# Kernel optimization log

Hardware: AMD Instinct MI355X
Metric: run time of the kernel (lower is better)

Reference implementation:

```python
import jax, jax.numpy as jnp
import numpy as np

B, S, D = 8, 1024, 1024
H, DH = 16, 64  # num_attention_heads, attention_head_size; H*DH == D


def setup_inputs() -> dict:
    key = jax.random.key(0)
    ks = jax.random.split(key, 6)
    scale = 0.02
    return {
        "hidden_states": jax.random.normal(ks[0], (B, S, D), jnp.float32),
        "right_hidden_states": jax.random.normal(ks[1], (B, S, D), jnp.float32),
        "attention_mask": jnp.ones((B, S, S), jnp.float32),
        "Wq": jax.random.normal(ks[2], (D, H * DH), jnp.float32) * scale,
        "bq": jnp.zeros((H * DH,), jnp.float32),
        "Wk": jax.random.normal(ks[3], (D, H * DH), jnp.float32) * scale,
        "bk": jnp.zeros((H * DH,), jnp.float32),
        "Wv": jax.random.normal(ks[4], (D, H * DH), jnp.float32) * scale,
        "bv": jnp.zeros((H * DH,), jnp.float32),
    }


def _split_heads(x, b):
    # (B, S, H*DH) -> (B, H, S, DH)
    return x.reshape(b, -1, H, DH).transpose(0, 2, 1, 3)


def reference(hidden_states, right_hidden_states, attention_mask, Wq, bq, Wk, bk, Wv, bv):
    b = hidden_states.shape[0]
    q = _split_heads(hidden_states @ Wq + bq, b)          # (B,H,Sq,DH)
    k = _split_heads(right_hidden_states @ Wk + bk, b)    # (B,H,Sk,DH)
    v = _split_heads(right_hidden_states @ Wv + bv, b)    # (B,H,Sk,DH)

    scores = jnp.einsum("bhqd,bhkd->bhqk", q, k) / jnp.sqrt(jnp.asarray(DH, q.dtype))
    scores = jnp.sum(scores, axis=1, keepdims=True)       # (B,1,Sq,Sk) head-summed

    ext = (1.0 - attention_mask[:, None, :, :].astype(scores.dtype)) * -1e9
    probs = jax.nn.softmax(scores + ext, axis=-1)         # (B,1,Sq,Sk)

    ctx = jnp.matmul(probs, v)                            # broadcast -> (B,H,Sq,DH)
    # Faithful to original: reshape WITHOUT transposing heads back.
    return ctx.reshape(b, -1, H * DH)                     # (B,Sq,H*DH)
```

## Files before the change

kernel.cpp:

```cpp
#include <hip/hip_runtime.h>
#include <stdint.h>

constexpr int S = 1024;
constexpr int D = 1024;
constexpr int NB = 8;

typedef __bf16 bf16x8 __attribute__((ext_vector_type(8)));
typedef float floatx4 __attribute__((ext_vector_type(4)));

#define AS1 __attribute__((address_space(1)))
#define AS3 __attribute__((address_space(3)))

__device__ __forceinline__ unsigned short f2bf(float f) {
  unsigned u = __builtin_bit_cast(unsigned, f);
  u += 0x7fffu + ((u >> 16) & 1u);
  return (unsigned short)(u >> 16);
}

__device__ __forceinline__ void gload16(const void* g, void* l) {
  __builtin_amdgcn_global_load_lds((const AS1 unsigned int*)g, (AS3 unsigned int*)l, 16, 0, 0);
}

__global__ __launch_bounds__(256) void prep_kernel(const float4* __restrict__ hs4,
                                                   const float4* __restrict__ rhs4,
                                                   ushort4* __restrict__ hsb4,
                                                   ushort4* __restrict__ rhsb4, int n4,
                                                   const float* __restrict__ Wq,
                                                   const float* __restrict__ Wk,
                                                   const float* __restrict__ Wv,
                                                   unsigned short* __restrict__ Wcat) {
  __shared__ float tile[32][33];
  const int bid = blockIdx.x;
  if (bid < 16384) {
    int i = bid * 256 + threadIdx.x;
    const float4* src;
    ushort4* dst;
    int j;
    if (i < n4) {
      src = hs4; dst = hsb4; j = i;
    } else {
      src = rhs4; dst = rhsb4; j = i - n4;
    }
    float4 v = src[j];
    ushort4 o;
    o.x = f2bf(v.x); o.y = f2bf(v.y); o.z = f2bf(v.z); o.w = f2bf(v.w);
    dst[j] = o;
  } else {
    const int t = bid - 16384;
    const int z = t >> 10;
    const int r = t & 1023;
    const float* W = (z == 0) ? Wq : (z == 1) ? Wk : Wv;
    unsigned short* Wt = Wcat + (long long)z * D * D;
    const int bx = (r & 31) * 32;
    const int by = (r >> 5) * 32;
    const int x = threadIdx.x & 31;
    const int y0 = threadIdx.x >> 5;
    for (int i = 0; i < 4; ++i) {
      int y = y0 + i * 8;
      tile[y][x] = W[(by + y) * D + bx + x];
    }
    __syncthreads();
    for (int i = 0; i < 4; ++i) {
      int y = y0 + i * 8;
      Wt[(long long)(bx + y) * D + by + x] = f2bf(tile[x][y]);
    }
  }
}


__global__ __launch_bounds__(256) void gemm_qkv_kernel(
    const unsigned short* __restrict__ hsb, const unsigned short* __restrict__ rhsb,
    const unsigned short* __restrict__ Wcat, unsigned short* __restrict__ Qm,
    unsigned short* __restrict__ Km, unsigned short* __restrict__ Vmt,
    const float* __restrict__ bq, const float* __restrict__ bk, const float* __restrict__ bv) {
  __shared__ __align__(16) unsigned short As[128 * 64];
  __shared__ __align__(16) unsigned short Bs[128 * 64];
  const int tid = threadIdx.x;
  const int lane = tid & 63;
  const int w = tid >> 6;
  const int bid = blockIdx.x;
  const int local = bid >> 3;
  const int n_tile = (bid & 7) * 3 + (local % 3);
  const long long m0 = (long long)(local / 3) * 128;
  const long long n0g = (long long)n_tile * 128;
  const int seg = n_tile >> 3;
  const unsigned short* A = (seg == 0) ? hsb : rhsb;
  const unsigned short* Bt = Wcat + n0g * D;
  const float* bias = (seg == 0) ? bq : (seg == 1) ? bk : bv;

  const unsigned short* aG[4];
  const unsigned short* bG[4];
  for (int j = 0; j < 4; ++j) {
    int idx = tid + j * 256;
    int row = idx >> 3;
    int cg = (idx & 7) ^ (row & 7);
    aG[j] = A + (m0 + row) * D + cg * 8;
    bG[j] = Bt + (long long)row * D + cg * 8;
  }

  floatx4 zero4 = {0.f, 0.f, 0.f, 0.f};
  floatx4 acc[4][4];
  for (int i = 0; i < 4; ++i)
    for (int j = 0; j < 4; ++j) acc[i][j] = zero4;

  const int r15 = lane & 15;
  const int quad = lane >> 4;
  const int wm = (w >> 1) * 64;
  const int wn = (w & 1) * 64;

  for (int k0 = 0; k0 < D; k0 += 64) {
    for (int j = 0; j < 4; ++j) gload16(aG[j] + k0, As + j * 2048 + w * 512);
    for (int j = 0; j < 4; ++j) gload16(bG[j] + k0, Bs + j * 2048 + w * 512);
    __syncthreads();
    for (int kk = 0; kk < 2; ++kk) {
      const int ca = ((kk << 2) | quad) ^ (r15 & 7);
      bf16x8 af[4], bfr[4];
      for (int t = 0; t < 4; ++t) {
        af[t] = *reinterpret_cast<const bf16x8*>(As + (wm + t * 16 + r15) * 64 + ca * 8);
        bfr[t] = *reinterpret_cast<const bf16x8*>(Bs + (wn + t * 16 + r15) * 64 + ca * 8);
      }
      for (int mt = 0; mt < 4; ++mt)
        for (int nt = 0; nt < 4; ++nt)
          acc[mt][nt] =
              __builtin_amdgcn_mfma_f32_16x16x32_bf16(af[mt], bfr[nt], acc[mt][nt], 0, 0, 0);
    }
    __syncthreads();
  }

  const long long nloc0 = n0g & 1023;
  for (int mt = 0; mt < 4; ++mt) {
    for (int nt = 0; nt < 4; ++nt) {
      const long long mrow = m0 + wm + mt * 16 + quad * 4;
      const long long nc = nloc0 + wn + nt * 16 + r15;
      const float bval = bias[nc];
      floatx4 v = acc[mt][nt];
      for (int e = 0; e < 4; ++e) {
        float val = v[e] + bval;
        long long m = mrow + e;
        if (seg == 0) {
          Qm[m * D + nc] = f2bf(val);
        } else if (seg == 1) {
          Km[m * D + nc] = f2bf(val);
        } else {
          Vmt[(m >> 10) * (long long)(S * D) + nc * S + (m & 1023)] = f2bf(val);
        }
      }
    }
  }
}

template <int MODE>
__global__ __launch_bounds__(256) void gemm_nt_kernel(
    const unsigned short* __restrict__ A, int lda, long long strideA,
    const unsigned short* __restrict__ Bt, int ldb, long long strideB, float* __restrict__ C,
    long long strideC, float alpha, int K) {
  __shared__ __align__(16) unsigned short As[128 * 64];
  __shared__ __align__(16) unsigned short Bs[128 * 64];
  const int tid = threadIdx.x;
  const int lane = tid & 63;
  const int w = tid >> 6;
  const int bid = blockIdx.x;
  const int z = bid & 7;
  const int local = bid >> 3;
  const long long m0 = (long long)(local & 7) * 128;
  const long long n0 = (long long)(local >> 3) * 128;
  A += (long long)z * strideA;
  Bt += (long long)z * strideB;

  const unsigned short* aG[4];
  const unsigned short* bG[4];
  for (int j = 0; j < 4; ++j) {
    int idx = tid + j * 256;
    int row = idx >> 3;
    int cg = (idx & 7) ^ (row & 7);
    aG[j] = A + (m0 + row) * lda + cg * 8;
    bG[j] = Bt + (n0 + row) * ldb + cg * 8;
  }

  floatx4 zero4 = {0.f, 0.f, 0.f, 0.f};
  floatx4 acc[4][4];
  for (int i = 0; i < 4; ++i)
    for (int j = 0; j < 4; ++j) acc[i][j] = zero4;

  const int r15 = lane & 15;
  const int quad = lane >> 4;
  const int wm = (w >> 1) * 64;
  const int wn = (w & 1) * 64;

  for (int k0 = 0; k0 < K; k0 += 64) {
    for (int j = 0; j < 4; ++j) gload16(aG[j] + k0, As + j * 2048 + w * 512);
    for (int j = 0; j < 4; ++j) gload16(bG[j] + k0, Bs + j * 2048 + w * 512);
    __syncthreads();
    for (int kk = 0; kk < 2; ++kk) {
      const int ca = ((kk << 2) | quad) ^ (r15 & 7);
      bf16x8 af[4], bfr[4];
      for (int t = 0; t < 4; ++t) {
        af[t] = *reinterpret_cast<const bf16x8*>(As + (wm + t * 16 + r15) * 64 + ca * 8);
        bfr[t] = *reinterpret_cast<const bf16x8*>(Bs + (wn + t * 16 + r15) * 64 + ca * 8);
      }
      for (int mt = 0; mt < 4; ++mt)
        for (int nt = 0; nt < 4; ++nt)
          acc[mt][nt] =
              __builtin_amdgcn_mfma_f32_16x16x32_bf16(af[mt], bfr[nt], acc[mt][nt], 0, 0, 0);
    }
    __syncthreads();
  }

  for (int mt = 0; mt < 4; ++mt) {
    for (int nt = 0; nt < 4; ++nt) {
      const long long mrow = m0 + wm + mt * 16 + quad * 4;
      const long long ncol = n0 + wn + nt * 16 + r15;
      floatx4 v = acc[mt][nt];
      for (int e = 0; e < 4; ++e) {
        float val = v[e] * alpha;
        long long m = mrow + e;
        if constexpr (MODE == 2) {
          C[(long long)z * strideC + m * S + ncol] = val;
        } else {
          C[(long long)z * strideC + (ncol >> 6) * (long long)(S * 64) + m * 64 + (ncol & 63)] =
              val;
        }
      }
    }
  }
}

__global__ __launch_bounds__(256) void softmax_kernel(const float* scores,
                                                      const float* __restrict__ mask,
                                                      unsigned short* probs) {
  const int bid = blockIdx.x;
  const long long row = (long long)(bid & 7) * 1024 + (bid >> 3);
  const float4* s4 = (const float4*)(scores + row * S);
  const float4* m4 = (const float4*)(mask + row * S);
  ushort4* p4 = (ushort4*)(probs + row * 2048);
  const int tid = threadIdx.x;
  const int lane = tid & 63, w = tid >> 6;
  float4 sv = s4[tid];
  float4 mv = m4[tid];
  float v[4] = {sv.x + (1.0f - mv.x) * -1e9f, sv.y + (1.0f - mv.y) * -1e9f,
                sv.z + (1.0f - mv.z) * -1e9f, sv.w + (1.0f - mv.w) * -1e9f};
  float mx = fmaxf(fmaxf(v[0], v[1]), fmaxf(v[2], v[3]));
  for (int off = 32; off; off >>= 1) mx = fmaxf(mx, __shfl_xor(mx, off, 64));
  __shared__ float redm[4], reds[4];
  if (lane == 0) redm[w] = mx;
  __syncthreads();
  mx = fmaxf(fmaxf(redm[0], redm[1]), fmaxf(redm[2], redm[3]));
  float sum = 0.f;
  for (int i = 0; i < 4; ++i) {
    v[i] = __expf(v[i] - mx);
    sum += v[i];
  }
  for (int off = 32; off; off >>= 1) sum += __shfl_xor(sum, off, 64);
  if (lane == 0) reds[w] = sum;
  __syncthreads();
  sum = reds[0] + reds[1] + reds[2] + reds[3];
  float inv = 1.0f / sum;
  ushort4 o;
  o.x = f2bf(v[0] * inv);
  o.y = f2bf(v[1] * inv);
  o.z = f2bf(v[2] * inv);
  o.w = f2bf(v[3] * inv);
  p4[tid] = o;
}

extern "C" void kernel_launch(void* const* d_in, const int* in_sizes, int n_in, void* d_out,
                              int out_size, void* d_ws, size_t ws_size, hipStream_t stream) {
  const float* hs = (const float*)d_in[0];
  const float* rhs = (const float*)d_in[1];
  const float* mask = (const float*)d_in[2];
  const float* Wq = (const float*)d_in[3];
  const float* bq = (const float*)d_in[4];
  const float* Wk = (const float*)d_in[5];
  const float* bk = (const float*)d_in[6];
  const float* Wv = (const float*)d_in[7];
  const float* bv = (const float*)d_in[8];
  float* out = (float*)d_out;
  char* ws = (char*)d_ws;
  const size_t MB = 1ull << 20;
  unsigned short* Wcat = (unsigned short*)(ws + 0 * MB);
  unsigned short* hsb = (unsigned short*)(ws + 6 * MB);
  unsigned short* rhsb = (unsigned short*)(ws + 22 * MB);
  unsigned short* Qm = (unsigned short*)(ws + 38 * MB);
  unsigned short* Km = (unsigned short*)(ws + 54 * MB);
  unsigned short* Vmt = (unsigned short*)(ws + 70 * MB);
  float* scores = (float*)(ws + 6 * MB);
  unsigned short* probs = (unsigned short*)scores;

  const int n4 = NB * S * D / 4;
  prep_kernel<<<16384 + 3072, 256, 0, stream>>>((const float4*)hs, (const float4*)rhs,
                                                (ushort4*)hsb, (ushort4*)rhsb, n4, Wq, Wk, Wv,
                                                Wcat);

  gemm_qkv_kernel<<<1536, 256, 0, stream>>>(hsb, rhsb, Wcat, Qm, Km, Vmt, bq, bk, bv);

  gemm_nt_kernel<2><<<512, 256, 0, stream>>>(Qm, D, (long long)S * D, Km, D, (long long)S * D,
                                             scores, (long long)S * S, 0.125f, D);
  softmax_kernel<<<NB * S, 256, 0, stream>>>(scores, mask, probs);
  gemm_nt_kernel<3><<<512, 256, 0, stream>>>(probs, 2048, (long long)S * 2048, Vmt, D,
                                             (long long)S * D, out, (long long)S * D, 1.f, D);
}
```

Baseline: 304.2 us.

## Register-prefetch GEMM tiles with K=32 stages instead of direct global-to-LDS loads

Both GEMM kernels drop the global_load_lds direct copies and instead load the next K=32 slice into registers while the current slice is computed, then store it into a smaller swizzled LDS buffer. The goal is to overlap global latency with MFMA work and halve LDS footprint, which can raise occupancy. In exchange there are twice as many barriers per K, extra VGPR use and a register round trip through LDS stores. The swizzle layout also changes, packing two rows per 64-element LDS line.

```diff
diff --git a/kernel.cpp b/kernel.cpp
--- a/kernel.cpp
+++ b/kernel.cpp
@@ -7,18 +7,12 @@
 
 typedef __bf16 bf16x8 __attribute__((ext_vector_type(8)));
 typedef float floatx4 __attribute__((ext_vector_type(4)));
-
-#define AS1 __attribute__((address_space(1)))
-#define AS3 __attribute__((address_space(3)))
+typedef unsigned short ushort8v __attribute__((ext_vector_type(8)));
 
 __device__ __forceinline__ unsigned short f2bf(float f) {
   unsigned u = __builtin_bit_cast(unsigned, f);
   u += 0x7fffu + ((u >> 16) & 1u);
   return (unsigned short)(u >> 16);
-}
-
-__device__ __forceinline__ void gload16(const void* g, void* l) {
-  __builtin_amdgcn_global_load_lds((const AS1 unsigned int*)g, (AS3 unsigned int*)l, 16, 0, 0);
 }
 
 __global__ __launch_bounds__(256) void prep_kernel(const float4* __restrict__ hs4,
@@ -68,13 +62,32 @@
 }
 
 
+#define GEMM_STAGE_ADDRS(Abase, lda_, Bbase, ldb_)                           \
+  const int srow0 = (tid >> 3) * 2 + ((tid >> 2) & 1);                       \
+  const int scol0 = (tid & 3) * 8;                                           \
+  const unsigned short* aG0 = (Abase) + (long long)(srow0) * (lda_) + scol0; \
+  const unsigned short* aG1 = aG0 + (long long)64 * (lda_);                  \
+  const unsigned short* bG0 = (Bbase) + (long long)(srow0) * (ldb_) + scol0; \
+  const unsigned short* bG1 = bG0 + (long long)64 * (ldb_);                  \
+  const int sr0 = tid >> 3;                                                  \
+  const int w0 = sr0 * 64 + (((tid & 7) ^ (sr0 & 7)) * 8);                   \
+  const int sr1 = sr0 + 32;                                                  \
+  const int w1 = sr1 * 64 + (((tid & 7) ^ (sr1 & 7)) * 8);
+
+#define GEMM_FRAG_READ(dst, Buf, wbase)                                      \
+  for (int t = 0; t < 4; ++t) {                                              \
+    int sr = ((wbase) + t * 16) / 2 + (r15 >> 1);                            \
+    int ch = p4q ^ (sr & 7);                                                 \
+    dst[t] = *reinterpret_cast<const bf16x8*>(Buf + sr * 64 + ch * 8);       \
+  }
+
 __global__ __launch_bounds__(256) void gemm_qkv_kernel(
     const unsigned short* __restrict__ hsb, const unsigned short* __restrict__ rhsb,
     const unsigned short* __restrict__ Wcat, unsigned short* __restrict__ Qm,
     unsigned short* __restrict__ Km, unsigned short* __restrict__ Vmt,
     const float* __restrict__ bq, const float* __restrict__ bk, const float* __restrict__ bv) {
-  __shared__ __align__(16) unsigned short As[128 * 64];
-  __shared__ __align__(16) unsigned short Bs[128 * 64];
+  __shared__ __align__(16) unsigned short As[128 * 32];
+  __shared__ __align__(16) unsigned short Bs[128 * 32];
   const int tid = threadIdx.x;
   const int lane = tid & 63;
   const int w = tid >> 6;
@@ -84,19 +97,11 @@
   const long long m0 = (long long)(local / 3) * 128;
   const long long n0g = (long long)n_tile * 128;
   const int seg = n_tile >> 3;
-  const unsigned short* A = (seg == 0) ? hsb : rhsb;
+  const unsigned short* A = ((seg == 0) ? hsb : rhsb) + m0 * D;
   const unsigned short* Bt = Wcat + n0g * D;
   const float* bias = (seg == 0) ? bq : (seg == 1) ? bk : bv;
 
-  const unsigned short* aG[4];
-  const unsigned short* bG[4];
-  for (int j = 0; j < 4; ++j) {
-    int idx = tid + j * 256;
-    int row = idx >> 3;
-    int cg = (idx & 7) ^ (row & 7);
-    aG[j] = A + (m0 + row) * D + cg * 8;
-    bG[j] = Bt + (long long)row * D + cg * 8;
-  }
+  GEMM_STAGE_ADDRS(A, D, Bt, D)
 
   floatx4 zero4 = {0.f, 0.f, 0.f, 0.f};
   floatx4 acc[4][4];
@@ -105,26 +110,32 @@
 
   const int r15 = lane & 15;
   const int quad = lane >> 4;
+  const int p4q = (r15 & 1) * 4 + quad;
   const int wm = (w >> 1) * 64;
   const int wn = (w & 1) * 64;
 
-  for (int k0 = 0; k0 < D; k0 += 64) {
-    for (int j = 0; j < 4; ++j) gload16(aG[j] + k0, As + j * 2048 + w * 512);
-    for (int j = 0; j < 4; ++j) gload16(bG[j] + k0, Bs + j * 2048 + w * 512);
-    __syncthreads();
-    for (int kk = 0; kk < 2; ++kk) {
-      const int ca = ((kk << 2) | quad) ^ (r15 & 7);
-      bf16x8 af[4], bfr[4];
-      for (int t = 0; t < 4; ++t) {
-        af[t] = *reinterpret_cast<const bf16x8*>(As + (wm + t * 16 + r15) * 64 + ca * 8);
-        bfr[t] = *reinterpret_cast<const bf16x8*>(Bs + (wn + t * 16 + r15) * 64 + ca * 8);
-      }
-      for (int mt = 0; mt < 4; ++mt)
-        for (int nt = 0; nt < 4; ++nt)
-          acc[mt][nt] =
-              __builtin_amdgcn_mfma_f32_16x16x32_bf16(af[mt], bfr[nt], acc[mt][nt], 0, 0, 0);
-    }
-    __syncthreads();
+  ushort8v sA0 = *(const ushort8v*)aG0, sA1 = *(const ushort8v*)aG1;
+  ushort8v sB0 = *(const ushort8v*)bG0, sB1 = *(const ushort8v*)bG1;
+  for (int k0 = 0; k0 < D; k0 += 32) {
+    __syncthreads();
+    *(ushort8v*)(As + w0) = sA0;
+    *(ushort8v*)(As + w1) = sA1;
+    *(ushort8v*)(Bs + w0) = sB0;
+    *(ushort8v*)(Bs + w1) = sB1;
+    __syncthreads();
+    if (k0 + 32 < D) {
+      sA0 = *(const ushort8v*)(aG0 + k0 + 32);
+      sA1 = *(const ushort8v*)(aG1 + k0 + 32);
+      sB0 = *(const ushort8v*)(bG0 + k0 + 32);
+      sB1 = *(const ushort8v*)(bG1 + k0 + 32);
+    }
+    bf16x8 af[4], bfr[4];
+    GEMM_FRAG_READ(af, As, wm)
+    GEMM_FRAG_READ(bfr, Bs, wn)
+    for (int mt = 0; mt < 4; ++mt)
+      for (int nt = 0; nt < 4; ++nt)
+        acc[mt][nt] =
+            __builtin_amdgcn_mfma_f32_16x16x32_bf16(af[mt], bfr[nt], acc[mt][nt], 0, 0, 0);
   }
 
   const long long nloc0 = n0g & 1023;
@@ -154,8 +165,8 @@
     const unsigned short* __restrict__ A, int lda, long long strideA,
     const unsigned short* __restrict__ Bt, int ldb, long long strideB, float* __restrict__ C,
     long long strideC, float alpha, int K) {
-  __shared__ __align__(16) unsigned short As[128 * 64];
-  __shared__ __align__(16) unsigned short Bs[128 * 64];
+  __shared__ __align__(16) unsigned short As[128 * 32];
+  __shared__ __align__(16) unsigned short Bs[128 * 32];
   const int tid = threadIdx.x;
   const int lane = tid & 63;
   const int w = tid >> 6;
@@ -164,18 +175,10 @@
   const int local = bid >> 3;
   const long long m0 = (long long)(local & 7) * 128;
   const long long n0 = (long long)(local >> 3) * 128;
-  A += (long long)z * strideA;
-  Bt += (long long)z * strideB;
-
-  const unsigned short* aG[4];
-  const unsigned short* bG[4];
-  for (int j = 0; j < 4; ++j) {
-    int idx = tid + j * 256;
-    int row = idx >> 3;
-    int cg = (idx & 7) ^ (row & 7);
-    aG[j] = A + (m0 + row) * lda + cg * 8;
-    bG[j] = Bt + (n0 + row) * ldb + cg * 8;
-  }
+  const unsigned short* Ab = A + (long long)z * strideA + m0 * lda;
+  const unsigned short* Bb = Bt + (long long)z * strideB + n0 * ldb;
+
+  GEMM_STAGE_ADDRS(Ab, lda, Bb, ldb)
 
   floatx4 zero4 = {0.f, 0.f, 0.f, 0.f};
   floatx4 acc[4][4];
@@ -184,26 +187,32 @@
 
   const int r15 = lane & 15;
   const int quad = lane >> 4;
+  const int p4q = (r15 & 1) * 4 + quad;
   const int wm = (w >> 1) * 64;
   const int wn = (w & 1) * 64;
 
-  for (int k0 = 0; k0 < K; k0 += 64) {
-    for (int j = 0; j < 4; ++j) gload16(aG[j] + k0, As + j * 2048 + w * 512);
-    for (int j = 0; j < 4; ++j) gload16(bG[j] + k0, Bs + j * 2048 + w * 512);
-    __syncthreads();
-    for (int kk = 0; kk < 2; ++kk) {
-      const int ca = ((kk << 2) | quad) ^ (r15 & 7);
-      bf16x8 af[4], bfr[4];
-      for (int t = 0; t < 4; ++t) {
-        af[t] = *reinterpret_cast<const bf16x8*>(As + (wm + t * 16 + r15) * 64 + ca * 8);
-        bfr[t] = *reinterpret_cast<const bf16x8*>(Bs + (wn + t * 16 + r15) * 64 + ca * 8);
-      }
-      for (int mt = 0; mt < 4; ++mt)
-        for (int nt = 0; nt < 4; ++nt)
-          acc[mt][nt] =
-              __builtin_amdgcn_mfma_f32_16x16x32_bf16(af[mt], bfr[nt], acc[mt][nt], 0, 0, 0);
-    }
-    __syncthreads();
+  ushort8v sA0 = *(const ushort8v*)aG0, sA1 = *(const ushort8v*)aG1;
+  ushort8v sB0 = *(const ushort8v*)bG0, sB1 = *(const ushort8v*)bG1;
+  for (int k0 = 0; k0 < K; k0 += 32) {
+    __syncthreads();
+    *(ushort8v*)(As + w0) = sA0;
+    *(ushort8v*)(As + w1) = sA1;
+    *(ushort8v*)(Bs + w0) = sB0;
+    *(ushort8v*)(Bs + w1) = sB1;
+    __syncthreads();
+    if (k0 + 32 < K) {
+      sA0 = *(const ushort8v*)(aG0 + k0 + 32);
+      sA1 = *(const ushort8v*)(aG1 + k0 + 32);
+      sB0 = *(const ushort8v*)(bG0 + k0 + 32);
+      sB1 = *(const ushort8v*)(bG1 + k0 + 32);
+    }
+    bf16x8 af[4], bfr[4];
+    GEMM_FRAG_READ(af, As, wm)
+    GEMM_FRAG_READ(bfr, Bs, wn)
+    for (int mt = 0; mt < 4; ++mt)
+      for (int nt = 0; nt < 4; ++nt)
+        acc[mt][nt] =
+            __builtin_amdgcn_mfma_f32_16x16x32_bf16(af[mt], bfr[nt], acc[mt][nt], 0, 0, 0);
   }
 
   for (int mt = 0; mt < 4; ++mt) {
```

New measurement: 316.1 us. +3.9%, slower.

## Double-buffer GEMM K-tiles in LDS and write probs to a dense separate buffer

Applied to the files above, without the earlier changes.

All three GEMM kernels now use two 32-wide K stages in LDS. The global-to-LDS load for the next stage is issued before the MFMAs on the current stage, so memory latency overlaps compute. The LDS footprint stays the same, with a new XOR swizzle for the 32-column rows. Softmax now writes bf16 probabilities into the Q buffer with a 1024 stride instead of aliasing the fp32 scores with a 2048 stride, so the restrict qualifiers are valid and the PV GEMM reads compact rows. The trade-off is more barriers per K step and a dependency on Q being dead by the time softmax runs.

```diff
diff --git a/kernel.cpp b/kernel.cpp
--- a/kernel.cpp
+++ b/kernel.cpp
@@ -68,13 +68,44 @@
 }
 
 
+#define GEMM_STAGE_SETUP(Abase, lda_, Bbase, ldb_)                                   \
+  const int lrow = w * 32 + ((tid & 63) >> 2);  \
+  const int csw = (((tid & 3) ^ ((lrow >> 1) & 3)) * 8);                              \
+  const unsigned short* aG0 = (Abase) + (long long)lrow * (lda_) + csw;               \
+  const unsigned short* aG1 = aG0 + (long long)16 * (lda_);                           \
+  const unsigned short* bG0 = (Bbase) + (long long)lrow * (ldb_) + csw;               \
+  const unsigned short* bG1 = bG0 + (long long)16 * (ldb_);                           \
+  unsigned short* aL0 = As + w * 1024;                                                \
+  unsigned short* aL1 = As + w * 1024 + 512;                                          \
+  unsigned short* bL0 = Bs + w * 1024;                                                \
+  unsigned short* bL1 = Bs + w * 1024 + 512;
+
+#define GEMM_STAGE(k0off, poff)          \
+  gload16(aG0 + (k0off), aL0 + (poff));  \
+  gload16(aG1 + (k0off), aL1 + (poff));  \
+  gload16(bG0 + (k0off), bL0 + (poff));  \
+  gload16(bG1 + (k0off), bL1 + (poff));
+
+#define GEMM_COMPUTE(poff)                                                            \
+  {                                                                                   \
+    bf16x8 af[4], bfr[4];                                                             \
+    for (int t = 0; t < 4; ++t) {                                                     \
+      af[t] = *reinterpret_cast<const bf16x8*>(As + (poff) + (wm + t * 16 + r15) * 32 + pq); \
+      bfr[t] = *reinterpret_cast<const bf16x8*>(Bs + (poff) + (wn + t * 16 + r15) * 32 + pq); \
+    }                                                                                 \
+    for (int mt = 0; mt < 4; ++mt)                                                    \
+      for (int nt = 0; nt < 4; ++nt)                                                  \
+        acc[mt][nt] =                                                                 \
+            __builtin_amdgcn_mfma_f32_16x16x32_bf16(af[mt], bfr[nt], acc[mt][nt], 0, 0, 0); \
+  }
+
 __global__ __launch_bounds__(256) void gemm_qkv_kernel(
     const unsigned short* __restrict__ hsb, const unsigned short* __restrict__ rhsb,
     const unsigned short* __restrict__ Wcat, unsigned short* __restrict__ Qm,
     unsigned short* __restrict__ Km, unsigned short* __restrict__ Vmt,
     const float* __restrict__ bq, const float* __restrict__ bk, const float* __restrict__ bv) {
-  __shared__ __align__(16) unsigned short As[128 * 64];
-  __shared__ __align__(16) unsigned short Bs[128 * 64];
+  __shared__ __align__(16) unsigned short As[2 * 4096];
+  __shared__ __align__(16) unsigned short Bs[2 * 4096];
   const int tid = threadIdx.x;
   const int lane = tid & 63;
   const int w = tid >> 6;
@@ -84,19 +115,11 @@
   const long long m0 = (long long)(local / 3) * 128;
   const long long n0g = (long long)n_tile * 128;
   const int seg = n_tile >> 3;
-  const unsigned short* A = (seg == 0) ? hsb : rhsb;
+  const unsigned short* A = ((seg == 0) ? hsb : rhsb) + m0 * D;
   const unsigned short* Bt = Wcat + n0g * D;
   const float* bias = (seg == 0) ? bq : (seg == 1) ? bk : bv;
 
-  const unsigned short* aG[4];
-  const unsigned short* bG[4];
-  for (int j = 0; j < 4; ++j) {
-    int idx = tid + j * 256;
-    int row = idx >> 3;
-    int cg = (idx & 7) ^ (row & 7);
-    aG[j] = A + (m0 + row) * D + cg * 8;
-    bG[j] = Bt + (long long)row * D + cg * 8;
-  }
+  GEMM_STAGE_SETUP(A, D, Bt, D)
 
   floatx4 zero4 = {0.f, 0.f, 0.f, 0.f};
   floatx4 acc[4][4];
@@ -105,26 +128,18 @@
 
   const int r15 = lane & 15;
   const int quad = lane >> 4;
+  const int pq = (quad ^ ((r15 >> 1) & 3)) * 8;
   const int wm = (w >> 1) * 64;
   const int wn = (w & 1) * 64;
 
+  GEMM_STAGE(0, 0)
   for (int k0 = 0; k0 < D; k0 += 64) {
-    for (int j = 0; j < 4; ++j) gload16(aG[j] + k0, As + j * 2048 + w * 512);
-    for (int j = 0; j < 4; ++j) gload16(bG[j] + k0, Bs + j * 2048 + w * 512);
-    __syncthreads();
-    for (int kk = 0; kk < 2; ++kk) {
-      const int ca = ((kk << 2) | quad) ^ (r15 & 7);
-      bf16x8 af[4], bfr[4];
-      for (int t = 0; t < 4; ++t) {
-        af[t] = *reinterpret_cast<const bf16x8*>(As + (wm + t * 16 + r15) * 64 + ca * 8);
-        bfr[t] = *reinterpret_cast<const bf16x8*>(Bs + (wn + t * 16 + r15) * 64 + ca * 8);
-      }
-      for (int mt = 0; mt < 4; ++mt)
-        for (int nt = 0; nt < 4; ++nt)
-          acc[mt][nt] =
-              __builtin_amdgcn_mfma_f32_16x16x32_bf16(af[mt], bfr[nt], acc[mt][nt], 0, 0, 0);
-    }
-    __syncthreads();
+    __syncthreads();
+    if (k0 + 32 < D) GEMM_STAGE(k0 + 32, 4096)
+    GEMM_COMPUTE(0)
+    __syncthreads();
+    if (k0 + 64 < D) GEMM_STAGE(k0 + 64, 0)
+    GEMM_COMPUTE(4096)
   }
 
   const long long nloc0 = n0g & 1023;
@@ -154,8 +169,8 @@
     const unsigned short* __restrict__ A, int lda, long long strideA,
     const unsigned short* __restrict__ Bt, int ldb, long long strideB, float* __restrict__ C,
     long long strideC, float alpha, int K) {
-  __shared__ __align__(16) unsigned short As[128 * 64];
-  __shared__ __align__(16) unsigned short Bs[128 * 64];
+  __shared__ __align__(16) unsigned short As[2 * 4096];
+  __shared__ __align__(16) unsigned short Bs[2 * 4096];
   const int tid = threadIdx.x;
   const int lane = tid & 63;
   const int w = tid >> 6;
@@ -164,18 +179,10 @@
   const int local = bid >> 3;
   const long long m0 = (long long)(local & 7) * 128;
   const long long n0 = (long long)(local >> 3) * 128;
-  A += (long long)z * strideA;
-  Bt += (long long)z * strideB;
-
-  const unsigned short* aG[4];
-  const unsigned short* bG[4];
-  for (int j = 0; j < 4; ++j) {
-    int idx = tid + j * 256;
-    int row = idx >> 3;
-    int cg = (idx & 7) ^ (row & 7);
-    aG[j] = A + (m0 + row) * lda + cg * 8;
-    bG[j] = Bt + (n0 + row) * ldb + cg * 8;
-  }
+  const unsigned short* Ab = A + (long long)z * strideA + m0 * lda;
+  const unsigned short* Bb = Bt + (long long)z * strideB + n0 * ldb;
+
+  GEMM_STAGE_SETUP(Ab, lda, Bb, ldb)
 
   floatx4 zero4 = {0.f, 0.f, 0.f, 0.f};
   floatx4 acc[4][4];
@@ -184,26 +191,18 @@
 
   const int r15 = lane & 15;
   const int quad = lane >> 4;
+  const int pq = (quad ^ ((r15 >> 1) & 3)) * 8;
   const int wm = (w >> 1) * 64;
   const int wn = (w & 1) * 64;
 
+  GEMM_STAGE(0, 0)
   for (int k0 = 0; k0 < K; k0 += 64) {
-    for (int j = 0; j < 4; ++j) gload16(aG[j] + k0, As + j * 2048 + w * 512);
-    for (int j = 0; j < 4; ++j) gload16(bG[j] + k0, Bs + j * 2048 + w * 512);
-    __syncthreads();
-    for (int kk = 0; kk < 2; ++kk) {
-      const int ca = ((kk << 2) | quad) ^ (r15 & 7);
-      bf16x8 af[4], bfr[4];
-      for (int t = 0; t < 4; ++t) {
-        af[t] = *reinterpret_cast<const bf16x8*>(As + (wm + t * 16 + r15) * 64 + ca * 8);
-        bfr[t] = *reinterpret_cast<const bf16x8*>(Bs + (wn + t * 16 + r15) * 64 + ca * 8);
-      }
-      for (int mt = 0; mt < 4; ++mt)
-        for (int nt = 0; nt < 4; ++nt)
-          acc[mt][nt] =
-              __builtin_amdgcn_mfma_f32_16x16x32_bf16(af[mt], bfr[nt], acc[mt][nt], 0, 0, 0);
-    }
-    __syncthreads();
+    __syncthreads();
+    if (k0 + 32 < K) GEMM_STAGE(k0 + 32, 4096)
+    GEMM_COMPUTE(0)
+    __syncthreads();
+    if (k0 + 64 < K) GEMM_STAGE(k0 + 64, 0)
+    GEMM_COMPUTE(4096)
   }
 
   for (int mt = 0; mt < 4; ++mt) {
@@ -225,14 +224,14 @@
   }
 }
 
-__global__ __launch_bounds__(256) void softmax_kernel(const float* scores,
+__global__ __launch_bounds__(256) void softmax_kernel(const float* __restrict__ scores,
                                                       const float* __restrict__ mask,
-                                                      unsigned short* probs) {
+                                                      unsigned short* __restrict__ probs) {
   const int bid = blockIdx.x;
   const long long row = (long long)(bid & 7) * 1024 + (bid >> 3);
   const float4* s4 = (const float4*)(scores + row * S);
   const float4* m4 = (const float4*)(mask + row * S);
-  ushort4* p4 = (ushort4*)(probs + row * 2048);
+  ushort4* p4 = (ushort4*)(probs + row * 1024);
   const int tid = threadIdx.x;
   const int lane = tid & 63, w = tid >> 6;
   float4 sv = s4[tid];
@@ -284,7 +283,7 @@
   unsigned short* Km = (unsigned short*)(ws + 54 * MB);
   unsigned short* Vmt = (unsigned short*)(ws + 70 * MB);
   float* scores = (float*)(ws + 6 * MB);
-  unsigned short* probs = (unsigned short*)scores;
+  unsigned short* probs = Qm;
 
   const int n4 = NB * S * D / 4;
   prep_kernel<<<16384 + 3072, 256, 0, stream>>>((const float4*)hs, (const float4*)rhs,
@@ -296,6 +295,6 @@
   gemm_nt_kernel<2><<<512, 256, 0, stream>>>(Qm, D, (long long)S * D, Km, D, (long long)S * D,
                                              scores, (long long)S * S, 0.125f, D);
   softmax_kernel<<<NB * S, 256, 0, stream>>>(scores, mask, probs);
-  gemm_nt_kernel<3><<<512, 256, 0, stream>>>(probs, 2048, (long long)S * 2048, Vmt, D,
+  gemm_nt_kernel<3><<<512, 256, 0, stream>>>(probs, 1024, (long long)S * 1024, Vmt, D,
                                              (long long)S * D, out, (long long)S * D, 1.f, D);
 }
```

After: 326.6 us. +7.4%, slower.
